# Performance work log

Measured on AMD Instinct MI355X. Metric: run time of the kernel, lower is better.

## Reference

```python
import jax, jax.numpy as jnp
import numpy as np

NEG = -1000000.0  # mask value used by the torch module


def setup_inputs() -> dict:
    key = jax.random.key(0)
    k1, k2, k3, k4 = jax.random.split(key, 4)
    B, Q, K, D = 16, 2048, 2048, 128
    queries = jax.random.normal(k1, (B, Q, D), dtype=jnp.float32)
    keys = jax.random.normal(k2, (B, K, D), dtype=jnp.float32)
    values = jax.random.normal(k3, (B, K, D), dtype=jnp.float32)
    valid_lens = jax.random.randint(k4, (B,), 0, K, dtype=jnp.int32)
    return {"queries": queries, "keys": keys, "values": values, "valid_lens": valid_lens}


def reference(queries, keys, values, valid_lens):
    d = queries.shape[-1]
    # scores: [B, Q, K]
    scores = jnp.einsum("bqd,bkd->bqk", queries, keys) / jnp.sqrt(jnp.float32(d))
    # mask key positions >= valid_len[b] with the same -1e6 value as torch
    kv_pos = jnp.arange(scores.shape[-1])  # [K]
    mask = kv_pos[None, None, :] < valid_lens[:, None, None]  # [B,1,K]
    scores = jnp.where(mask, scores, NEG)
    attn = jax.nn.softmax(scores, axis=-1)
    # dropout p=0.0 -> identity (module in eval)
    return jnp.einsum("bqk,bkd->bqd", attn, values)
```

## Files before the change

### kernel.cpp

```cpp
#include <hip/hip_runtime.h>
#include <hip/hip_bf16.h>

#define NB    16
#define NQ    2048
#define NKV   2048
#define DH    128
#define KVT   64
#define NTILE 32
#define TILE_BYTES 16384
#define TILE_ELT   8192

typedef __attribute__((ext_vector_type(8))) short short8;
typedef __attribute__((ext_vector_type(4))) float f32x4;

__device__ __forceinline__ unsigned short f2bf(float f) {
    union { float f; unsigned int u; } x; x.f = f;
    unsigned int r = (x.u + 0x7fffu + ((x.u >> 16) & 1u)) >> 16;
    return (unsigned short)r;
}

__device__ __forceinline__ void load_lds16(const void* g, void* l) {
    __builtin_amdgcn_global_load_lds(
        (const __attribute__((address_space(1))) unsigned int*)g,
        (__attribute__((address_space(3))) unsigned int*)l, 16, 0, 0);
}

__global__ __launch_bounds__(256)
void preconv(const float* __restrict__ kg, const float* __restrict__ vg,
             const int* __restrict__ vlg,
             unsigned short* __restrict__ kws, unsigned short* __restrict__ vws) {
    __shared__ __align__(16) unsigned short lv[TILE_ELT];
    const int tid = threadIdx.x;
    const int rb = (blockIdx.x & 7) * 64 + (blockIdx.x >> 3);
    const int b = rb >> 5, t = rb & 31;
    const int vl = vlg[b];
    const int ntiles = (vl == 0) ? NTILE : ((vl + KVT - 1) >> 6);
    if (t >= ntiles) return;

    const float* kb = kg + ((size_t)b * NKV + t * KVT) * DH;
    const float* vb = vg + ((size_t)b * NKV + t * KVT) * DH;
    char* kimg = (char*)(kws + (size_t)(b * NTILE + t) * TILE_ELT);
    char* vimg = (char*)(vws + (size_t)(b * NTILE + t) * TILE_ELT);

    #pragma unroll
    for (int p = 0; p < 4; ++p) {
        int idx = p * 256 + tid;
        int row = idx >> 4, ch = idx & 15;
        f32x4 a = *(const f32x4*)(kb + row * DH + ch * 8);
        f32x4 c = *(const f32x4*)(kb + row * DH + ch * 8 + 4);
        union { short8 v; unsigned short u[8]; } w;
        #pragma unroll
        for (int j = 0; j < 4; ++j) { w.u[j] = f2bf(a[j]); w.u[4 + j] = f2bf(c[j]); }
        *(short8*)(kimg + row * 256 + ((ch * 16) ^ ((row & 7) << 4))) = w.v;
        f32x4 va = *(const f32x4*)(vb + row * DH + ch * 8);
        f32x4 vc = *(const f32x4*)(vb + row * DH + ch * 8 + 4);
        union { short8 v; unsigned short u[8]; } w2;
        #pragma unroll
        for (int j = 0; j < 4; ++j) { w2.u[j] = f2bf(va[j]); w2.u[4 + j] = f2bf(vc[j]); }
        *(short8*)((char*)lv + row * 256 + ((ch * 16) ^ (((row >> 3) & 7) << 4))) = w2.v;
    }
    __syncthreads();
    #pragma unroll
    for (int p = 0; p < 4; ++p) {
        int task = p * 256 + tid;
        int c = task & 7, d = task >> 3;
        union { short8 v; unsigned short u[8]; } w;
        #pragma unroll
        for (int j = 0; j < 8; ++j) {
            int kv = c * 8 + j;
            w.u[j] = *(const unsigned short*)((const char*)lv + kv * 256 + ((d * 2) ^ (((kv >> 3) & 7) << 4)));
        }
        *(short8*)(vimg + d * 128 + ((c * 16) ^ ((d & 7) << 4))) = w.v;
    }
}

__global__ __launch_bounds__(128, 2)
void attn_fwd3(const float* __restrict__ qg,
               const unsigned short* __restrict__ kws,
               const unsigned short* __restrict__ vws,
               const int* __restrict__ vlg, float* __restrict__ og) {
    __shared__ __align__(16) unsigned short lds_k[TILE_ELT];
    __shared__ __align__(16) unsigned short lds_v[TILE_ELT];
    __shared__ __align__(16) unsigned short lds_p[2][16 * KVT];

    const int tid = threadIdx.x;
    const int lane = tid & 63;
    const int wv = tid >> 6;
    const int row16 = lane & 15;
    const int g = lane >> 4;

    const int bid = blockIdx.x;
    const int b  = bid & 15;
    const int qt = bid >> 4;
    const int q0 = qt * 32 + wv * 16;
    const int vl = vlg[b];

    const float QS = 1.4426950408889634f * 0.08838834764831845f;
    short8 qf[4];
    {
        const float* qp = qg + ((size_t)b * NQ + q0 + row16) * DH + g * 8;
        #pragma unroll
        for (int c = 0; c < 4; ++c) {
            f32x4 a  = *(const f32x4*)(qp + c * 32);
            f32x4 bb = *(const f32x4*)(qp + c * 32 + 4);
            union { short8 v; unsigned short u[8]; } t;
            #pragma unroll
            for (int j = 0; j < 4; ++j) { t.u[j] = f2bf(a[j] * QS); t.u[4 + j] = f2bf(bb[j] * QS); }
            qf[c] = t.v;
        }
    }

    const int ntiles = (vl == 0) ? NTILE : ((vl + KVT - 1) >> 6);
    const float MASKV = (vl == 0) ? 0.0f : -1442695.0f;

    f32x4 oacc[8];
    f32x4 ellacc = (f32x4){0.f, 0.f, 0.f, 0.f};
    #pragma unroll
    for (int n = 0; n < 8; ++n) oacc[n] = (f32x4){0.f, 0.f, 0.f, 0.f};
    short8 ones;
    {
        union { short8 v; unsigned short u[8]; } t;
        #pragma unroll
        for (int j = 0; j < 8; ++j) t.u[j] = 0x3F80;
        ones = t.v;
    }

    const char* kbase = (const char*)kws + (size_t)b * NTILE * TILE_BYTES;
    const char* vbase = (const char*)vws + (size_t)b * NTILE * TILE_BYTES;

    for (int tt = 0; tt < ntiles; ++tt) {
        __syncthreads();
        const char* ks = kbase + (size_t)tt * TILE_BYTES;
        const char* vs = vbase + (size_t)tt * TILE_BYTES;
        #pragma unroll
        for (int i = 0; i < 8; ++i) {
            int off = i * 2048 + wv * 1024;
            load_lds16(ks + off + lane * 16, (char*)lds_k + off);
            load_lds16(vs + off + lane * 16, (char*)lds_v + off);
        }
        asm volatile("s_waitcnt vmcnt(0)" ::: "memory");
        __syncthreads();

        f32x4 s[4];
        __builtin_amdgcn_s_setprio(1);
        #pragma unroll
        for (int n = 0; n < 4; ++n) {
            s[n] = (f32x4){0.f, 0.f, 0.f, 0.f};
            int krow = n * 16 + row16;
            #pragma unroll
            for (int c = 0; c < 4; ++c) {
                short8 kf = *(const short8*)((const char*)lds_k + krow * 256 +
                                             ((c * 64 + g * 16) ^ ((krow & 7) << 4)));
                s[n] = __builtin_amdgcn_mfma_f32_16x16x32_bf16(qf[c], kf, s[n], 0, 0, 0);
            }
        }
        __builtin_amdgcn_s_setprio(0);

        if (vl == 0 || tt == ntiles - 1) {
            int kvb = tt * KVT;
            #pragma unroll
            for (int n = 0; n < 4; ++n) {
                if (kvb + n * 16 + row16 >= vl) {
                    #pragma unroll
                    for (int r = 0; r < 4; ++r) s[n][r] = MASKV;
                }
            }
        }

        #pragma unroll
        for (int n = 0; n < 4; ++n) {
            #pragma unroll
            for (int r = 0; r < 4; ++r) {
                float p = __builtin_amdgcn_exp2f(s[n][r]);
                int qr = g * 4 + r;
                int swz = (g ^ (r << 1)) & 7;
                __hip_bfloat16 h = __float2bfloat16(p);
                *(unsigned short*)((char*)lds_p[wv] + qr * 128 +
                                   (((n * 16 + row16) * 2) ^ (swz << 4))) =
                    *reinterpret_cast<unsigned short*>(&h);
            }
        }
        asm volatile("s_waitcnt lgkmcnt(0)" ::: "memory");

        const int swzr = ((row16 >> 2) ^ ((row16 & 3) << 1)) & 7;
        __builtin_amdgcn_s_setprio(1);
        #pragma unroll
        for (int kc = 0; kc < 2; ++kc) {
            short8 pf = *(const short8*)((const char*)lds_p[wv] + row16 * 128 +
                                         ((kc * 64 + g * 16) ^ (swzr << 4)));
            ellacc = __builtin_amdgcn_mfma_f32_16x16x32_bf16(pf, ones, ellacc, 0, 0, 0);
            #pragma unroll
            for (int n2 = 0; n2 < 8; ++n2) {
                int vrow = n2 * 16 + row16;
                short8 vf = *(const short8*)((const char*)lds_v + vrow * 128 +
                                             ((kc * 64 + g * 16) ^ ((vrow & 7) << 4)));
                oacc[n2] = __builtin_amdgcn_mfma_f32_16x16x32_bf16(pf, vf, oacc[n2], 0, 0, 0);
            }
        }
        __builtin_amdgcn_s_setprio(0);
    }

    float* ob = og + ((size_t)b * NQ + q0) * DH;
    float rl[4];
    #pragma unroll
    for (int r = 0; r < 4; ++r) rl[r] = 1.0f / ellacc[r];
    #pragma unroll
    for (int n2 = 0; n2 < 8; ++n2) {
        #pragma unroll
        for (int r = 0; r < 4; ++r)
            ob[(size_t)(g * 4 + r) * DH + n2 * 16 + row16] = oacc[n2][r] * rl[r];
    }
}

extern "C" void kernel_launch(void* const* d_in, const int* in_sizes, int n_in,
                              void* d_out, int out_size, void* d_ws, size_t ws_size,
                              hipStream_t stream) {
    const float* q  = (const float*)d_in[0];
    const float* k  = (const float*)d_in[1];
    const float* v  = (const float*)d_in[2];
    const int*   vl = (const int*)d_in[3];
    float* o = (float*)d_out;

    unsigned short* kws = (unsigned short*)d_ws;
    unsigned short* vws = (unsigned short*)((char*)d_ws + (size_t)NB * NTILE * TILE_BYTES);
    preconv<<<dim3(NB * NTILE), dim3(256), 0, stream>>>(k, v, vl, kws, vws);
    attn_fwd3<<<dim3(NB * 64), dim3(128), 0, stream>>>(q, kws, vws, vl, o);
}
```

Before: 69.90 us.

## Rewrite attention with 32x32 MFMA, double-buffered KV tiles, and split-KV combine

Replaces the 16x16 MFMA attention kernel with one that uses 32x32x16 bf16 MFMAs over 32-key tiles. Each wave now owns 32 query rows, P is kept in registers through permlane32 swaps instead of being staged in LDS, and the next K/V tile is prefetched into a second LDS buffer. Work can be split across S KV partitions, which writes bf16 partial outputs and row sums that a new combine kernel reduces. The split is meant to raise parallelism and the double buffering to hide load latency, at the cost of extra workspace traffic, bf16 rounding of the partials, and a third kernel launch.

```diff
diff --git a/kernel.cpp b/kernel.cpp
--- a/kernel.cpp
+++ b/kernel.cpp
@@ -5,13 +5,15 @@
 #define NQ    2048
 #define NKV   2048
 #define DH    128
-#define KVT   64
-#define NTILE 32
-#define TILE_BYTES 16384
-#define TILE_ELT   8192
-
-typedef __attribute__((ext_vector_type(8))) short short8;
-typedef __attribute__((ext_vector_type(4))) float f32x4;
+#define KVT   32
+#define NT    64
+#define TIMG  8192
+
+typedef __attribute__((ext_vector_type(8)))  short  short8;
+typedef __attribute__((ext_vector_type(4)))  float  f32x4;
+typedef __attribute__((ext_vector_type(2)))  float  f32x2;
+typedef __attribute__((ext_vector_type(16))) float  f32x16;
+typedef __attribute__((ext_vector_type(2)))  unsigned int u32x2;
 
 __device__ __forceinline__ unsigned short f2bf(float f) {
     union { float f; unsigned int u; } x; x.f = f;
@@ -19,6 +21,10 @@
     return (unsigned short)r;
 }
 
+__device__ __forceinline__ float u2f(unsigned int u) {
+    union { unsigned int u; float f; } x; x.u = u; return x.f;
+}
+
 __device__ __forceinline__ void load_lds16(const void* g, void* l) {
     __builtin_amdgcn_global_load_lds(
         (const __attribute__((address_space(1))) unsigned int*)g,
@@ -27,189 +33,242 @@
 
 __global__ __launch_bounds__(256)
 void preconv(const float* __restrict__ kg, const float* __restrict__ vg,
-             const int* __restrict__ vlg,
-             unsigned short* __restrict__ kws, unsigned short* __restrict__ vws) {
-    __shared__ __align__(16) unsigned short lv[TILE_ELT];
+             const int* __restrict__ vlg, char* __restrict__ kws,
+             char* __restrict__ vws) {
     const int tid = threadIdx.x;
-    const int rb = (blockIdx.x & 7) * 64 + (blockIdx.x >> 3);
-    const int b = rb >> 5, t = rb & 31;
+    const int bid = blockIdx.x;
+    const int b = bid & 15, t = bid >> 4;
     const int vl = vlg[b];
-    const int ntiles = (vl == 0) ? NTILE : ((vl + KVT - 1) >> 6);
-    if (t >= ntiles) return;
+    const int nt = (vl == 0) ? NT : ((vl + KVT - 1) >> 5);
+    if (t >= nt) return;
 
     const float* kb = kg + ((size_t)b * NKV + t * KVT) * DH;
     const float* vb = vg + ((size_t)b * NKV + t * KVT) * DH;
-    char* kimg = (char*)(kws + (size_t)(b * NTILE + t) * TILE_ELT);
-    char* vimg = (char*)(vws + (size_t)(b * NTILE + t) * TILE_ELT);
+    char* kimg = kws + (size_t)(b * NT + t) * TIMG;
+    char* vimg = vws + (size_t)(b * NT + t) * TIMG;
 
     #pragma unroll
-    for (int p = 0; p < 4; ++p) {
+    for (int p = 0; p < 2; ++p) {
         int idx = p * 256 + tid;
-        int row = idx >> 4, ch = idx & 15;
-        f32x4 a = *(const f32x4*)(kb + row * DH + ch * 8);
-        f32x4 c = *(const f32x4*)(kb + row * DH + ch * 8 + 4);
+        int kv = idx >> 4, ch = idx & 15;
+        f32x4 a = *(const f32x4*)(kb + kv * DH + ch * 8);
+        f32x4 c = *(const f32x4*)(kb + kv * DH + ch * 8 + 4);
         union { short8 v; unsigned short u[8]; } w;
         #pragma unroll
         for (int j = 0; j < 4; ++j) { w.u[j] = f2bf(a[j]); w.u[4 + j] = f2bf(c[j]); }
-        *(short8*)(kimg + row * 256 + ((ch * 16) ^ ((row & 7) << 4))) = w.v;
-        f32x4 va = *(const f32x4*)(vb + row * DH + ch * 8);
-        f32x4 vc = *(const f32x4*)(vb + row * DH + ch * 8 + 4);
-        union { short8 v; unsigned short u[8]; } w2;
-        #pragma unroll
-        for (int j = 0; j < 4; ++j) { w2.u[j] = f2bf(va[j]); w2.u[4 + j] = f2bf(vc[j]); }
-        *(short8*)((char*)lv + row * 256 + ((ch * 16) ^ (((row >> 3) & 7) << 4))) = w2.v;
-    }
-    __syncthreads();
+        *(short8*)(kimg + kv * 256 + ((ch * 16) ^ ((kv & 15) << 4))) = w.v;
+    }
     #pragma unroll
-    for (int p = 0; p < 4; ++p) {
+    for (int p = 0; p < 2; ++p) {
         int task = p * 256 + tid;
-        int c = task & 7, d = task >> 3;
-        union { short8 v; unsigned short u[8]; } w;
-        #pragma unroll
-        for (int j = 0; j < 8; ++j) {
-            int kv = c * 8 + j;
-            w.u[j] = *(const unsigned short*)((const char*)lv + kv * 256 + ((d * 2) ^ (((kv >> 3) & 7) << 4)));
-        }
-        *(short8*)(vimg + d * 128 + ((c * 16) ^ ((d & 7) << 4))) = w.v;
-    }
-}
-
-__global__ __launch_bounds__(128, 2)
-void attn_fwd3(const float* __restrict__ qg,
-               const unsigned short* __restrict__ kws,
-               const unsigned short* __restrict__ vws,
-               const int* __restrict__ vlg, float* __restrict__ og) {
-    __shared__ __align__(16) unsigned short lds_k[TILE_ELT];
-    __shared__ __align__(16) unsigned short lds_v[TILE_ELT];
-    __shared__ __align__(16) unsigned short lds_p[2][16 * KVT];
-
-    const int tid = threadIdx.x;
+        int w = task & 3, d = task >> 2;
+        union { short8 v; unsigned short u[8]; } o;
+        #pragma unroll
+        for (int j = 0; j < 8; ++j) o.u[j] = f2bf(vb[(w * 8 + j) * DH + d]);
+        int byte = (d >> 2) * 256 + 16 * ((w + 4 * (d & 3)) ^ ((d >> 2) & 15));
+        *(short8*)(vimg + byte) = o.v;
+    }
+}
+
+__global__ __launch_bounds__(256, 3)
+void attn32(const float* __restrict__ qg, const char* __restrict__ kws,
+            const char* __restrict__ vws, const int* __restrict__ vlg,
+            float* __restrict__ og, unsigned int* __restrict__ opart,
+            float* __restrict__ ellg, int S) {
+    __shared__ __align__(16) char smem[32768];
+
+    const int tid  = threadIdx.x;
     const int lane = tid & 63;
-    const int wv = tid >> 6;
-    const int row16 = lane & 15;
-    const int g = lane >> 4;
+    const int wv   = tid >> 6;
+    const int l31  = lane & 31;
+    const int h    = lane >> 5;
 
     const int bid = blockIdx.x;
     const int b  = bid & 15;
-    const int qt = bid >> 4;
-    const int q0 = qt * 32 + wv * 16;
+    const int qt = (bid >> 4) & 15;
+    const int s  = bid >> 8;
+    const int q0 = qt * 128 + wv * 32;
     const int vl = vlg[b];
+    const int nt = (vl == 0) ? NT : ((vl + KVT - 1) >> 5);
+
+    if (s >= nt) {
+        if (S > 1 && tid < 128)
+            ellg[(size_t)s * NB * NQ + (size_t)b * NQ + qt * 128 + tid] = 0.f;
+        return;
+    }
 
     const float QS = 1.4426950408889634f * 0.08838834764831845f;
-    short8 qf[4];
+    short8 qw[8];
     {
-        const float* qp = qg + ((size_t)b * NQ + q0 + row16) * DH + g * 8;
-        #pragma unroll
-        for (int c = 0; c < 4; ++c) {
-            f32x4 a  = *(const f32x4*)(qp + c * 32);
-            f32x4 bb = *(const f32x4*)(qp + c * 32 + 4);
+        const float* qp = qg + ((size_t)b * NQ + q0 + l31) * DH + h * 8;
+        #pragma unroll
+        for (int c = 0; c < 8; ++c) {
+            f32x4 a  = *(const f32x4*)(qp + c * 16);
+            f32x4 bb = *(const f32x4*)(qp + c * 16 + 4);
             union { short8 v; unsigned short u[8]; } t;
             #pragma unroll
             for (int j = 0; j < 4; ++j) { t.u[j] = f2bf(a[j] * QS); t.u[4 + j] = f2bf(bb[j] * QS); }
-            qf[c] = t.v;
-        }
-    }
-
-    const int ntiles = (vl == 0) ? NTILE : ((vl + KVT - 1) >> 6);
+            qw[c] = t.v;
+        }
+    }
+
     const float MASKV = (vl == 0) ? 0.0f : -1442695.0f;
-
-    f32x4 oacc[8];
-    f32x4 ellacc = (f32x4){0.f, 0.f, 0.f, 0.f};
+    f32x16 oacc[4];
     #pragma unroll
-    for (int n = 0; n < 8; ++n) oacc[n] = (f32x4){0.f, 0.f, 0.f, 0.f};
-    short8 ones;
-    {
-        union { short8 v; unsigned short u[8]; } t;
-        #pragma unroll
-        for (int j = 0; j < 8; ++j) t.u[j] = 0x3F80;
-        ones = t.v;
-    }
-
-    const char* kbase = (const char*)kws + (size_t)b * NTILE * TILE_BYTES;
-    const char* vbase = (const char*)vws + (size_t)b * NTILE * TILE_BYTES;
-
-    for (int tt = 0; tt < ntiles; ++tt) {
-        __syncthreads();
-        const char* ks = kbase + (size_t)tt * TILE_BYTES;
-        const char* vs = vbase + (size_t)tt * TILE_BYTES;
-        #pragma unroll
-        for (int i = 0; i < 8; ++i) {
-            int off = i * 2048 + wv * 1024;
-            load_lds16(ks + off + lane * 16, (char*)lds_k + off);
-            load_lds16(vs + off + lane * 16, (char*)lds_v + off);
-        }
+    for (int d = 0; d < 4; ++d) oacc[d] = (f32x16)(0.0f);
+    float esum = 0.f;
+
+    const char* kbase = kws + (size_t)b * NT * TIMG;
+    const char* vbase = vws + (size_t)b * NT * TIMG;
+
+    auto issue = [&](int t, int pb) {
+        const char* ks = kbase + (size_t)t * TIMG;
+        const char* vs = vbase + (size_t)t * TIMG;
+        char* kd = smem + pb * 8192;
+        char* vd = smem + 16384 + pb * 8192;
+        #pragma unroll
+        for (int i = 0; i < 2; ++i) {
+            int off = wv * 2048 + i * 1024;
+            load_lds16(ks + off + lane * 16, kd + off);
+        }
+        #pragma unroll
+        for (int i = 0; i < 2; ++i) {
+            int off = wv * 2048 + i * 1024;
+            load_lds16(vs + off + lane * 16, vd + off);
+        }
+    };
+
+    issue(s, 0);
+    int p = 0;
+    const int l15s = (l31 & 15) << 4;
+
+    for (int tt = s; tt < nt; tt += S) {
         asm volatile("s_waitcnt vmcnt(0)" ::: "memory");
         __syncthreads();
-
-        f32x4 s[4];
+        int tn = tt + S;
+        if (tn < nt) issue(tn, p ^ 1);
+
+        const char* kb = smem + p * 8192;
+        const char* vb = smem + 16384 + p * 8192;
+
+        f32x16 sc = (f32x16)(0.0f);
         __builtin_amdgcn_s_setprio(1);
         #pragma unroll
-        for (int n = 0; n < 4; ++n) {
-            s[n] = (f32x4){0.f, 0.f, 0.f, 0.f};
-            int krow = n * 16 + row16;
+        for (int c = 0; c < 8; ++c) {
+            short8 kf = *(const short8*)(kb + l31 * 256 + ((c * 32 + h * 16) ^ l15s));
+            sc = __builtin_amdgcn_mfma_f32_32x32x16_bf16(kf, qw[c], sc, 0, 0, 0);
+        }
+        __builtin_amdgcn_s_setprio(0);
+
+        if (vl == 0 || tt == nt - 1) {
+            int kvb = tt * 32 + 4 * h;
             #pragma unroll
-            for (int c = 0; c < 4; ++c) {
-                short8 kf = *(const short8*)((const char*)lds_k + krow * 256 +
-                                             ((c * 64 + g * 16) ^ ((krow & 7) << 4)));
-                s[n] = __builtin_amdgcn_mfma_f32_16x16x32_bf16(qf[c], kf, s[n], 0, 0, 0);
+            for (int r = 0; r < 16; ++r) {
+                int kvg = kvb + (r & 3) + 8 * (r >> 2);
+                if (kvg >= vl) sc[r] = MASKV;
             }
         }
+
+        float pe[16];
+        #pragma unroll
+        for (int r = 0; r < 16; ++r) pe[r] = __builtin_amdgcn_exp2f(sc[r]);
+        esum += (((pe[0] + pe[1]) + (pe[2] + pe[3])) + ((pe[4] + pe[5]) + (pe[6] + pe[7])))
+              + (((pe[8] + pe[9]) + (pe[10] + pe[11])) + ((pe[12] + pe[13]) + (pe[14] + pe[15])));
+
+        unsigned int A, B, C, D, E, F, G, H;
+        asm("v_cvt_pk_bf16_f32 %0, %1, %2" : "=v"(A) : "v"(pe[0]),  "v"(pe[1]));
+        asm("v_cvt_pk_bf16_f32 %0, %1, %2" : "=v"(B) : "v"(pe[2]),  "v"(pe[3]));
+        asm("v_cvt_pk_bf16_f32 %0, %1, %2" : "=v"(C) : "v"(pe[4]),  "v"(pe[5]));
+        asm("v_cvt_pk_bf16_f32 %0, %1, %2" : "=v"(D) : "v"(pe[6]),  "v"(pe[7]));
+        asm("v_cvt_pk_bf16_f32 %0, %1, %2" : "=v"(E) : "v"(pe[8]),  "v"(pe[9]));
+        asm("v_cvt_pk_bf16_f32 %0, %1, %2" : "=v"(F) : "v"(pe[10]), "v"(pe[11]));
+        asm("v_cvt_pk_bf16_f32 %0, %1, %2" : "=v"(G) : "v"(pe[12]), "v"(pe[13]));
+        asm("v_cvt_pk_bf16_f32 %0, %1, %2" : "=v"(H) : "v"(pe[14]), "v"(pe[15]));
+        asm("v_permlane32_swap_b32 %0, %1" : "+v"(A), "+v"(C));
+        asm("v_permlane32_swap_b32 %0, %1" : "+v"(B), "+v"(D));
+        asm("v_permlane32_swap_b32 %0, %1" : "+v"(E), "+v"(G));
+        asm("v_permlane32_swap_b32 %0, %1" : "+v"(F), "+v"(H));
+        union { short8 v; unsigned int w[4]; } P0, P1;
+        P0.w[0] = A; P0.w[1] = B; P0.w[2] = C; P0.w[3] = D;
+        P1.w[0] = E; P1.w[1] = F; P1.w[2] = G; P1.w[3] = H;
+        short8 pa[2] = { P0.v, P1.v };
+
+        __builtin_amdgcn_s_setprio(1);
+        #pragma unroll
+        for (int dblk = 0; dblk < 4; ++dblk) {
+            int quad = dblk * 8 + (l31 >> 2);
+            int xk = quad & 15;
+            #pragma unroll
+            for (int c16 = 0; c16 < 2; ++c16) {
+                int w = c16 * 2 + h;
+                short8 vf = *(const short8*)(vb + quad * 256 +
+                                             16 * ((w + 4 * (l31 & 3)) ^ xk));
+                oacc[dblk] = __builtin_amdgcn_mfma_f32_32x32x16_bf16(vf, pa[c16], oacc[dblk], 0, 0, 0);
+            }
+        }
         __builtin_amdgcn_s_setprio(0);
-
-        if (vl == 0 || tt == ntiles - 1) {
-            int kvb = tt * KVT;
-            #pragma unroll
-            for (int n = 0; n < 4; ++n) {
-                if (kvb + n * 16 + row16 >= vl) {
-                    #pragma unroll
-                    for (int r = 0; r < 4; ++r) s[n][r] = MASKV;
-                }
+        p ^= 1;
+    }
+
+    float ea = esum, eb;
+    asm volatile("v_mov_b32 %0, %1" : "=v"(eb) : "v"(esum));
+    asm("v_permlane32_swap_b32 %0, %1" : "+v"(ea), "+v"(eb));
+    float ell = ea + eb;
+
+    __syncthreads();
+
+    if (S > 1 && lane < 32)
+        ellg[(size_t)s * NB * NQ + (size_t)b * NQ + q0 + lane] = ell;
+
+    float* tw = (float*)smem + wv * 1120;
+    if (lane < 32) tw[1088 + l31] = 1.0f / ell;
+    unsigned int* opw = opart + ((size_t)s * NB * NQ + (size_t)b * NQ + q0) * 64;
+    float* ogp = og + ((size_t)b * NQ + q0) * DH;
+
+    #pragma unroll
+    for (int dblk = 0; dblk < 4; ++dblk) {
+        #pragma unroll
+        for (int r = 0; r < 16; ++r) {
+            int dd = (r & 3) + 8 * (r >> 2) + 4 * h;
+            tw[l31 * 34 + dd] = oacc[dblk][r];
+        }
+        #pragma unroll
+        for (int pp = 0; pp < 8; ++pp) {
+            int qq = pp * 4 + (lane >> 4);
+            int cc = lane & 15;
+            f32x2 v = *(f32x2*)(tw + qq * 34 + cc * 2);
+            if (S == 1) {
+                float rl = tw[1088 + qq];
+                f32x2 o = { v[0] * rl, v[1] * rl };
+                *(f32x2*)(ogp + (size_t)qq * DH + dblk * 32 + cc * 2) = o;
+            } else {
+                unsigned int w;
+                asm("v_cvt_pk_bf16_f32 %0, %1, %2" : "=v"(w) : "v"(v[0]), "v"(v[1]));
+                opw[(size_t)qq * 64 + dblk * 16 + cc] = w;
             }
         }
-
-        #pragma unroll
-        for (int n = 0; n < 4; ++n) {
-            #pragma unroll
-            for (int r = 0; r < 4; ++r) {
-                float p = __builtin_amdgcn_exp2f(s[n][r]);
-                int qr = g * 4 + r;
-                int swz = (g ^ (r << 1)) & 7;
-                __hip_bfloat16 h = __float2bfloat16(p);
-                *(unsigned short*)((char*)lds_p[wv] + qr * 128 +
-                                   (((n * 16 + row16) * 2) ^ (swz << 4))) =
-                    *reinterpret_cast<unsigned short*>(&h);
-            }
-        }
-        asm volatile("s_waitcnt lgkmcnt(0)" ::: "memory");
-
-        const int swzr = ((row16 >> 2) ^ ((row16 & 3) << 1)) & 7;
-        __builtin_amdgcn_s_setprio(1);
-        #pragma unroll
-        for (int kc = 0; kc < 2; ++kc) {
-            short8 pf = *(const short8*)((const char*)lds_p[wv] + row16 * 128 +
-                                         ((kc * 64 + g * 16) ^ (swzr << 4)));
-            ellacc = __builtin_amdgcn_mfma_f32_16x16x32_bf16(pf, ones, ellacc, 0, 0, 0);
-            #pragma unroll
-            for (int n2 = 0; n2 < 8; ++n2) {
-                int vrow = n2 * 16 + row16;
-                short8 vf = *(const short8*)((const char*)lds_v + vrow * 128 +
-                                             ((kc * 64 + g * 16) ^ ((vrow & 7) << 4)));
-                oacc[n2] = __builtin_amdgcn_mfma_f32_16x16x32_bf16(pf, vf, oacc[n2], 0, 0, 0);
-            }
-        }
-        __builtin_amdgcn_s_setprio(0);
-    }
-
-    float* ob = og + ((size_t)b * NQ + q0) * DH;
-    float rl[4];
-    #pragma unroll
-    for (int r = 0; r < 4; ++r) rl[r] = 1.0f / ellacc[r];
-    #pragma unroll
-    for (int n2 = 0; n2 < 8; ++n2) {
-        #pragma unroll
-        for (int r = 0; r < 4; ++r)
-            ob[(size_t)(g * 4 + r) * DH + n2 * 16 + row16] = oacc[n2][r] * rl[r];
-    }
+    }
+}
+
+__global__ __launch_bounds__(256)
+void combine(const unsigned int* __restrict__ opart, const float* __restrict__ ellg,
+             float* __restrict__ og, int S) {
+    int idx = blockIdx.x * 256 + threadIdx.x;
+    int row = idx >> 5;
+    int c   = idx & 31;
+    float a0 = 0.f, a1 = 0.f, a2 = 0.f, a3 = 0.f, l = 0.f;
+    for (int s = 0; s < S; ++s) {
+        float le = ellg[(size_t)s * NB * NQ + row];
+        if (le != 0.f) {
+            l += le;
+            u32x2 w = *(const u32x2*)(opart + ((size_t)s * NB * NQ + row) * 64 + c * 2);
+            a0 += u2f(w[0] << 16); a1 += u2f(w[0] & 0xffff0000u);
+            a2 += u2f(w[1] << 16); a3 += u2f(w[1] & 0xffff0000u);
+        }
+    }
+    float rl = 1.0f / l;
+    f32x4 o = { a0 * rl, a1 * rl, a2 * rl, a3 * rl };
+    *(f32x4*)(og + (size_t)row * DH + c * 4) = o;
 }
 
 extern "C" void kernel_launch(void* const* d_in, const int* in_sizes, int n_in,
@@ -221,8 +280,23 @@
     const int*   vl = (const int*)d_in[3];
     float* o = (float*)d_out;
 
-    unsigned short* kws = (unsigned short*)d_ws;
-    unsigned short* vws = (unsigned short*)((char*)d_ws + (size_t)NB * NTILE * TILE_BYTES);
-    preconv<<<dim3(NB * NTILE), dim3(256), 0, stream>>>(k, v, vl, kws, vws);
-    attn_fwd3<<<dim3(NB * 64), dim3(128), 0, stream>>>(q, kws, vws, vl, o);
-}
+    const size_t IMG     = (size_t)NB * NT * TIMG;
+    const size_t ELL_OFF = 2 * IMG;
+    const size_t ELL_MAX = (size_t)4 * NB * NQ * 4;
+    const size_t OP_OFF  = ELL_OFF + ELL_MAX;
+    const size_t OP_ONE  = (size_t)NB * NQ * DH * 2;
+
+    int S = 1;
+    if (ws_size >= OP_OFF + 4 * OP_ONE) S = 4;
+    else if (ws_size >= OP_OFF + 2 * OP_ONE) S = 2;
+
+    char* kws = (char*)d_ws;
+    char* vws = (char*)d_ws + IMG;
+    float* ellg = (float*)((char*)d_ws + ELL_OFF);
+    unsigned int* opart = (unsigned int*)((char*)d_ws + OP_OFF);
+
+    preconv<<<dim3(NB * NT), dim3(256), 0, stream>>>(k, v, vl, kws, vws);
+    attn32<<<dim3(256 * S), dim3(256), 0, stream>>>(q, kws, vws, vl, o, opart, ellg, S);
+    if (S > 1)
+        combine<<<dim3(NB * NQ * 32 / 256), dim3(256), 0, stream>>>(opart, ellg, o, S);
+}
```

Result: faster. 61.37 us (-12.2%).
